# Kernel optimization log

Measured on AMD Instinct MI355X. Metric: run time of the kernel, lower is better.

## Reference

```python
import jax, jax.numpy as jnp
import numpy as np

BN_EPS = 1e-5


def setup_inputs() -> dict:
    key = jax.random.key(0)
    ks = jax.random.split(key, 11)
    C, P = 256, 128  # inplanes, planes = inplanes // 2
    B, H, W = 4, 64, 64
    s = 0.01  # conv weight init std in the original module
    return {
        "x": jax.random.normal(ks[0], (B, C, H, W), jnp.float32),
        "Wt": jax.random.normal(ks[1], (P, C), jnp.float32) * s,
        "bt": jnp.zeros((P,), jnp.float32),
        "Wp": jax.random.normal(ks[2], (P, C), jnp.float32) * s,
        "bp": jnp.zeros((P,), jnp.float32),
        "Wg": jax.random.normal(ks[3], (P, C), jnp.float32) * s,
        "bg": jnp.zeros((P,), jnp.float32),
        "Wz": jax.random.normal(ks[4], (C, P), jnp.float32) * s,
        "bz": jnp.zeros((C,), jnp.float32),
        "gamma": jax.random.uniform(ks[5], (C,), jnp.float32),
        "beta": jax.random.normal(ks[6], (C,), jnp.float32) * 0.01,
    }


def reference(x, Wt, bt, Wp, bp, Wg, bg, Wz, bz, gamma, beta):
    b, c, h, w = x.shape
    n = h * w
    xf = x.reshape(b, c, n)  # (b, c, n)
    # 1x1 conv projections == per-pixel matmuls
    t = jnp.einsum("pc,bcn->bnp", Wt, xf) + bt            # (b, n, p) queries
    p = jnp.einsum("pc,bcn->bpn", Wp, xf) + bp[:, None]   # (b, p, n) keys
    g = jnp.einsum("pc,bcn->bnp", Wg, xf) + bg            # (b, n, p) values
    planes = Wt.shape[0]
    scale = jnp.asarray(planes, x.dtype) ** 0.5
    att = jnp.einsum("bnp,bpm->bnm", t, p) / scale        # (b, n, n)
    att = jax.nn.softmax(att, axis=-1)                    # softmax over dim 2
    y = jnp.einsum("bnm,bmp->bnp", att, g)                # (b, n, p)
    z = jnp.einsum("cp,bnp->bcn", Wz, y) + bz[:, None]    # (b, c, n)
    z = z.reshape(b, c, h, w)
    # BatchNorm2d, training-mode batch statistics over (B, H, W)
    mean = z.mean(axis=(0, 2, 3))
    var = z.var(axis=(0, 2, 3))
    zn = (z - mean[:, None, None]) * jax.lax.rsqrt(var + BN_EPS)[:, None, None]
    out = zn * gamma[:, None, None] + beta[:, None, None] + x
    return out
```

## Files before the change

kernel.cpp:

```cpp
#include <hip/hip_runtime.h>


#define SCALE_ 0.08838834764831845f

typedef __bf16 bf16x8 __attribute__((ext_vector_type(8)));
typedef float f32x4 __attribute__((ext_vector_type(4)));
typedef unsigned short ushort8v __attribute__((ext_vector_type(8)));

__device__ inline unsigned short f2bf(float f) {
  unsigned int u = __float_as_uint(f);
  u += 0x7fffu + ((u >> 16) & 1u);
  return (unsigned short)(u >> 16);
}
__device__ inline float bflo(unsigned int u) { return __uint_as_float(u << 16); }
__device__ inline float bfhi(unsigned int u) { return __uint_as_float(u & 0xffff0000u); }

__device__ inline void gl16(const unsigned short* g, unsigned short* l) {
  __builtin_amdgcn_global_load_lds(
      (const __attribute__((address_space(1))) unsigned int*)(g),
      (__attribute__((address_space(3))) unsigned int*)(l), 16, 0, 0);
}

__global__ __launch_bounds__(256) void prep_kernel(
    const float* __restrict__ x,
    const float* __restrict__ Wt, const float* __restrict__ Wp, const float* __restrict__ Wg,
    unsigned short* __restrict__ xT, unsigned short* __restrict__ Wb) {
  const int tid = threadIdx.x;
  const int bx = blockIdx.x, b = blockIdx.y;
  if (bx >= 64) {
    if (b != 0) return;
#pragma unroll
    for (int it = 0; it < 3; ++it) {
      int k = (bx - 64) * 256 + tid + it * 4096;
      const float* src = (k < 4096 ? Wt : (k < 8192 ? Wp : Wg)) + (size_t)(k & 4095) * 8;
      float4 a = *(const float4*)src, c = *(const float4*)(src + 4);
      ushort8v us;
      us[0] = f2bf(a.x); us[1] = f2bf(a.y); us[2] = f2bf(a.z); us[3] = f2bf(a.w);
      us[4] = f2bf(c.x); us[5] = f2bf(c.y); us[6] = f2bf(c.z); us[7] = f2bf(c.w);
      *(ushort8v*)(Wb + (size_t)k * 8) = us;
    }
    return;
  }
  __shared__ float sT[128 * 68];
  const int w = tid >> 6, l = tid & 63;
  const int n0 = bx * 64;
  for (int half = 0; half < 2; ++half) {
    if (half) __syncthreads();
#pragma unroll
    for (int it = 0; it < 8; ++it) {
      int e = it * 256 + tid;
      int c = e >> 4, n4 = e & 15;
      float4 v = *(const float4*)(x + (size_t)(b * 256 + half * 128 + c) * 4096 + n0 + n4 * 4);
      *(float4*)(sT + c * 68 + n4 * 4) = v;
    }
    __syncthreads();
#pragma unroll
    for (int it = 0; it < 4; ++it) {
      int c8 = it * 4 + w;
      int n = l;
      ushort8v us;
#pragma unroll
      for (int j = 0; j < 8; ++j) us[j] = f2bf(sT[(c8 * 8 + j) * 68 + n]);
      *(ushort8v*)(xT + (size_t)b * 1048576 + (size_t)(n0 + n) * 256 + half * 128 + c8 * 8) = us;
    }
  }
}

__global__ __launch_bounds__(256, 3) void proj_kernel(
    const unsigned short* __restrict__ xT, const unsigned short* __restrict__ Wb,
    const float* __restrict__ bt, const float* __restrict__ bp, const float* __restrict__ bg,
    unsigned short* __restrict__ Qb, unsigned short* __restrict__ Kb,
    unsigned short* __restrict__ Vtb) {
  __shared__ unsigned short sX[64 * 256];
  __shared__ unsigned short sW[128 * 64];
  const int tid = threadIdx.x;
  const int w = tid >> 6, l = tid & 63;
  const int l15 = l & 15, lh = l >> 4;
  const int n0 = blockIdx.x * 64;
  const int b = blockIdx.y;
  const int sel = blockIdx.z;
  const unsigned short* xTb = xT + (size_t)b * 1048576;
  const unsigned short* Ws = Wb + (size_t)sel * 32768;
#pragma unroll
  for (int it = 0; it < 8; ++it) {
    int row = w * 16 + it * 2 + (l >> 5);
    int s = l & 31;
    int src = (s & 24) | ((s & 7) ^ (row & 7));
    gl16(xTb + (size_t)(n0 + row) * 256 + src * 8, sX + (w * 16 + it * 2) * 256);
  }
  f32x4 acc[2][4];
#pragma unroll
  for (int mt = 0; mt < 2; ++mt)
#pragma unroll
    for (int nt = 0; nt < 4; ++nt) acc[mt][nt] = (f32x4){0.f, 0.f, 0.f, 0.f};

  for (int ko4 = 0; ko4 < 4; ++ko4) {
    __syncthreads();
#pragma unroll
    for (int it = 0; it < 4; ++it) {
      int p = w * 32 + it * 8 + (l >> 3);
      int s = l & 7;
      gl16(Ws + (size_t)p * 256 + ko4 * 64 + ((s ^ (p & 7)) * 8),
           sW + (w * 32 + it * 8) * 64);
    }
    __syncthreads();
#pragma unroll
    for (int ko2 = 0; ko2 < 2; ++ko2) {
      bf16x8 af[2];
#pragma unroll
      for (int mt = 0; mt < 2; ++mt) {
        int p = w * 32 + mt * 16 + l15;
        af[mt] = *(const bf16x8*)(sW + p * 64 + (((ko2 * 4 + lh) ^ (p & 7)) << 3));
      }
#pragma unroll
      for (int nt = 0; nt < 4; ++nt) {
        int n = nt * 16 + l15;
        int ci = ko4 * 8 + ko2 * 4 + lh;
        int slot = (ci & 24) | ((ci & 7) ^ (n & 7));
        bf16x8 bfv = *(const bf16x8*)(sX + n * 256 + (slot << 3));
#pragma unroll
        for (int mt = 0; mt < 2; ++mt)
          acc[mt][nt] = __builtin_amdgcn_mfma_f32_16x16x32_bf16(af[mt], bfv, acc[mt][nt], 0, 0, 0);
      }
    }
  }
  const float* bias = sel == 0 ? bt : (sel == 1 ? bp : bg);
  const float scl = sel == 0 ? SCALE_ : 1.0f;
#pragma unroll
  for (int mt = 0; mt < 2; ++mt) {
    int pb = w * 32 + mt * 16 + lh * 4;
    float4 bv = *(const float4*)(bias + pb);
    const float* bvf = (const float*)&bv;
    if (sel < 2) {
      unsigned short* dst = (sel == 0 ? Qb : Kb) + (size_t)b * 524288;
#pragma unroll
      for (int nt = 0; nt < 4; ++nt) {
        ushort4 us;
        us.x = f2bf((acc[mt][nt][0] + bv.x) * scl);
        us.y = f2bf((acc[mt][nt][1] + bv.y) * scl);
        us.z = f2bf((acc[mt][nt][2] + bv.z) * scl);
        us.w = f2bf((acc[mt][nt][3] + bv.w) * scl);
        *(ushort4*)(dst + (size_t)(n0 + nt * 16 + l15) * 128 + pb) = us;
      }
    } else {
      unsigned short* dst = Vtb + (size_t)b * 524288;
#pragma unroll
      for (int nt = 0; nt < 4; ++nt)
#pragma unroll
        for (int r = 0; r < 4; ++r)
          dst[(size_t)(pb + r) * 4096 + n0 + nt * 16 + l15] = f2bf(acc[mt][nt][r] + bvf[r]);
    }
  }
}

__global__ __launch_bounds__(256, 4) void attn_kernel(
    const unsigned short* __restrict__ Qb, const unsigned short* __restrict__ Kb,
    const unsigned short* __restrict__ Vtb, unsigned short* __restrict__ Ytp,
    float* __restrict__ denp) {
  __shared__ unsigned short sm[18432];
  const int tid = threadIdx.x;
  const int w = tid >> 6, l = tid & 63;
  const int l15 = l & 15, lh = l >> 4;
  const int b = blockIdx.y, sp = blockIdx.z;
  const int n0 = blockIdx.x * 64;
  const int kvbase = sp * 1024;

  bf16x8 qf[4];
  {
    const unsigned short* qrow = Qb + (size_t)(b * 4096 + n0 + w * 16 + l15) * 128 + lh * 8;
#pragma unroll
    for (int ko = 0; ko < 4; ++ko) qf[ko] = *(const bf16x8*)(qrow + ko * 32);
  }
  unsigned short* sPw = sm + 16384 + w * 512;

  f32x4 yacc[8];
#pragma unroll
  for (int i = 0; i < 8; ++i) yacc[i] = (f32x4){0.f, 0.f, 0.f, 0.f};
  float den = 0.f;

  const unsigned short* Kbase = Kb + (size_t)(b * 4096 + kvbase) * 128;
  const unsigned short* Vbase = Vtb + (size_t)(b * 128) * 4096 + kvbase;

#define STAGE(T, BUFO)                                                              \
  {                                                                                 \
    const int koff_ = (T) * 32;                                                     \
    _Pragma("unroll")                                                               \
    for (int it = 0; it < 2; ++it) {                                                \
      int krow = w * 8 + it * 4 + (l >> 4);                                         \
      gl16(Kbase + (size_t)(koff_ + krow) * 128 + (((l & 15) ^ (krow & 7)) << 3),   \
           sm + (BUFO) + (w * 8 + it * 4) * 128);                                   \
      int vrow = w * 32 + it * 16 + (l >> 2);                                       \
      gl16(Vbase + (size_t)vrow * 4096 + koff_ + (((l & 3) ^ (vrow & 3)) << 3),     \
           sm + 8192 + (BUFO) + (w * 32 + it * 16) * 32);                           \
    }                                                                               \
  }

  STAGE(0, 0)
  for (int t = 0; t < 32; ++t) {
    const int co = (t & 1) * 4096;
    unsigned short* kb = sm + co;
    unsigned short* vb = sm + 8192 + co;
    __syncthreads();
    if (t + 1 < 32) {
      STAGE(t + 1, co ^ 4096)
    }
    f32x4 sacc[2];
#pragma unroll
    for (int mt = 0; mt < 2; ++mt) sacc[mt] = (f32x4){0.f, 0.f, 0.f, 0.f};
    __builtin_amdgcn_s_setprio(1);
#pragma unroll
    for (int ko = 0; ko < 4; ++ko) {
#pragma unroll
      for (int mt = 0; mt < 2; ++mt) {
        int m = mt * 16 + l15;
        bf16x8 ak = *(const bf16x8*)(kb + m * 128 + (((lh + 4 * ko) ^ (m & 7)) << 3));
        sacc[mt] = __builtin_amdgcn_mfma_f32_16x16x32_bf16(ak, qf[ko], sacc[mt], 0, 0, 0);
      }
    }
    __builtin_amdgcn_s_setprio(0);
    float rs = 0.f;
#pragma unroll
    for (int mt = 0; mt < 2; ++mt) {
      float e0 = __expf(sacc[mt][0]);
      float e1 = __expf(sacc[mt][1]);
      float e2 = __expf(sacc[mt][2]);
      float e3 = __expf(sacc[mt][3]);
      rs += (e0 + e1) + (e2 + e3);
      ushort4 us;
      us.x = f2bf(e0); us.y = f2bf(e1); us.z = f2bf(e2); us.w = f2bf(e3);
      int bk = mt * 2 + (lh >> 1);
      *(ushort4*)(sPw + l15 * 32 + ((bk ^ (l15 & 3)) << 3) + (lh & 1) * 4) = us;
    }
    rs += __shfl_xor(rs, 16);
    rs += __shfl_xor(rs, 32);
    den += rs;
    bf16x8 bp = *(const bf16x8*)(sPw + l15 * 32 + ((lh ^ (l15 & 3)) << 3));
    __builtin_amdgcn_s_setprio(1);
#pragma unroll
    for (int dt = 0; dt < 8; ++dt) {
      int d = dt * 16 + l15;
      bf16x8 av = *(const bf16x8*)(vb + d * 32 + ((lh ^ (d & 3)) << 3));
      yacc[dt] = __builtin_amdgcn_mfma_f32_16x16x32_bf16(av, bp, yacc[dt], 0, 0, 0);
    }
    __builtin_amdgcn_s_setprio(0);
  }
  unsigned short* Yt = Ytp + (size_t)(sp * 4 + b) * 524288 +
                       (size_t)(n0 + w * 16 + l15) * 128;
#pragma unroll
  for (int dt = 0; dt < 8; ++dt) {
    ushort4 us;
    us.x = f2bf(yacc[dt][0]); us.y = f2bf(yacc[dt][1]);
    us.z = f2bf(yacc[dt][2]); us.w = f2bf(yacc[dt][3]);
    *(ushort4*)(Yt + dt * 16 + lh * 4) = us;
  }
  if (lh == 0) denp[(size_t)(sp * 4 + b) * 4096 + n0 + w * 16 + l15] = den;
}

__global__ __launch_bounds__(256, 4) void zbn_kernel(
    const unsigned short* __restrict__ Ytp, const float* __restrict__ denp,
    const float* __restrict__ Wz, const float* __restrict__ bz,
    float* __restrict__ Z, float* __restrict__ S1p, float* __restrict__ S2p) {
  __shared__ unsigned short sY[64 * 128];
  __shared__ unsigned short sW[64 * 128];
  __shared__ float sDen[64];
  const int tid = threadIdx.x;
  const int w = tid >> 6, l = tid & 63;
  const int l15 = l & 15, lh = l >> 4;
  const int bx = blockIdx.x;
  const int b = blockIdx.y;
  const int n0 = bx * 64;
  const int c0 = blockIdx.z * 64;
  if (tid < 64) {
    float s = 0.f;
#pragma unroll
    for (int sp = 0; sp < 4; ++sp) s += denp[sp * 16384 + b * 4096 + n0 + tid];
    sDen[tid] = 1.0f / s;
  }
  __syncthreads();
#pragma unroll
  for (int it = 0; it < 4; ++it) {
    int e = it * 256 + tid;
    int n = e >> 4, pc = e & 15;
    size_t o = (size_t)b * 524288 + (size_t)(n0 + n) * 128 + pc * 8;
    float a0 = 0, a1 = 0, a2 = 0, a3 = 0, a4 = 0, a5 = 0, a6 = 0, a7 = 0;
#pragma unroll
    for (int sp = 0; sp < 4; ++sp) {
      uint4 v = *(const uint4*)(Ytp + (size_t)sp * 2097152 + o);
      a0 += bflo(v.x); a1 += bfhi(v.x);
      a2 += bflo(v.y); a3 += bfhi(v.y);
      a4 += bflo(v.z); a5 += bfhi(v.z);
      a6 += bflo(v.w); a7 += bfhi(v.w);
    }
    float idn = sDen[n];
    ushort8v us;
    us[0] = f2bf(a0 * idn); us[1] = f2bf(a1 * idn);
    us[2] = f2bf(a2 * idn); us[3] = f2bf(a3 * idn);
    us[4] = f2bf(a4 * idn); us[5] = f2bf(a5 * idn);
    us[6] = f2bf(a6 * idn); us[7] = f2bf(a7 * idn);
    *(ushort8v*)(sY + n * 128 + ((pc ^ (n & 7)) << 3)) = us;
  }
#pragma unroll
  for (int it = 0; it < 4; ++it) {
    int e = it * 256 + tid;
    int c = e >> 4, pc = e & 15;
    const float* wsrc = Wz + (size_t)(c0 + c) * 128 + pc * 8;
    float4 wa = *(const float4*)(wsrc);
    float4 wb = *(const float4*)(wsrc + 4);
    ushort8v us;
    us[0] = f2bf(wa.x); us[1] = f2bf(wa.y); us[2] = f2bf(wa.z); us[3] = f2bf(wa.w);
    us[4] = f2bf(wb.x); us[5] = f2bf(wb.y); us[6] = f2bf(wb.z); us[7] = f2bf(wb.w);
    *(ushort8v*)(sW + c * 128 + ((pc ^ (c & 7)) << 3)) = us;
  }
  __syncthreads();
  f32x4 acc[4];
#pragma unroll
  for (int nt = 0; nt < 4; ++nt) acc[nt] = (f32x4){0.f, 0.f, 0.f, 0.f};
  const int crow = w * 16 + l15;
#pragma unroll
  for (int ko = 0; ko < 4; ++ko) {
    bf16x8 aw = *(const bf16x8*)(sW + crow * 128 + (((lh + 4 * ko) ^ (crow & 7)) << 3));
#pragma unroll
    for (int nt = 0; nt < 4; ++nt) {
      int nrow = nt * 16 + l15;
      bf16x8 by = *(const bf16x8*)(sY + nrow * 128 + (((lh + 4 * ko) ^ (nrow & 7)) << 3));
      acc[nt] = __builtin_amdgcn_mfma_f32_16x16x32_bf16(aw, by, acc[nt], 0, 0, 0);
    }
  }
  const int cb = c0 + w * 16 + lh * 4;
  float4 bzv = *(const float4*)(bz + cb);
  const float* bzf = (const float*)&bzv;
#pragma unroll
  for (int r = 0; r < 4; ++r) {
    float s1 = 0.f, s2 = 0.f;
#pragma unroll
    for (int nt = 0; nt < 4; ++nt) {
      float z = acc[nt][r] + bzf[r];
      Z[(size_t)(b * 256 + cb + r) * 4096 + n0 + nt * 16 + l15] = z;
      s1 += z;
      s2 += z * z;
    }
#pragma unroll
    for (int m = 1; m < 16; m <<= 1) {
      s1 += __shfl_xor(s1, m);
      s2 += __shfl_xor(s2, m);
    }
    if (l15 == 0) {
      S1p[(size_t)(cb + r) * 256 + b * 64 + bx] = s1;
      S2p[(size_t)(cb + r) * 256 + b * 64 + bx] = s2;
    }
  }
}

__global__ __launch_bounds__(256) void bnfin_kernel(
    const float* __restrict__ S1p, const float* __restrict__ S2p,
    const float* __restrict__ gamma, const float* __restrict__ beta,
    float* __restrict__ Scale, float* __restrict__ Shift) {
  __shared__ float r1[4], r2[4];
  const int c = blockIdx.x, tid = threadIdx.x;
  float s1 = S1p[(size_t)c * 256 + tid];
  float s2 = S2p[(size_t)c * 256 + tid];
#pragma unroll
  for (int m = 1; m < 64; m <<= 1) {
    s1 += __shfl_xor(s1, m);
    s2 += __shfl_xor(s2, m);
  }
  if ((tid & 63) == 0) { r1[tid >> 6] = s1; r2[tid >> 6] = s2; }
  __syncthreads();
  if (tid == 0) {
    float S1t = (r1[0] + r1[1]) + (r1[2] + r1[3]);
    float S2t = (r2[0] + r2[1]) + (r2[2] + r2[3]);
    const float inv_cnt = 1.0f / 16384.0f;
    float mean = S1t * inv_cnt;
    float var = fmaxf(S2t * inv_cnt - mean * mean, 0.0f);
    float inv = rsqrtf(var + 1e-5f);
    float sc = gamma[c] * inv;
    Scale[c] = sc;
    Shift[c] = beta[c] - mean * sc;
  }
}

__global__ __launch_bounds__(256) void out_kernel(
    const float* __restrict__ Z, const float* __restrict__ x,
    const float* __restrict__ Scale, const float* __restrict__ Shift,
    float* __restrict__ out) {
  int i4 = blockIdx.x * 256 + threadIdx.x;
  int flat = i4 << 2;
  int c = (flat >> 12) & 255;
  float4 z = *(const float4*)(Z + flat);
  float4 xv = *(const float4*)(x + flat);
  float sc = Scale[c], sh = Shift[c];
  float4 o;
  o.x = z.x * sc + sh + xv.x;
  o.y = z.y * sc + sh + xv.y;
  o.z = z.z * sc + sh + xv.z;
  o.w = z.w * sc + sh + xv.w;
  *(float4*)(out + flat) = o;
}

extern "C" void kernel_launch(void* const* d_in, const int* in_sizes, int n_in,
                              void* d_out, int out_size, void* d_ws, size_t ws_size,
                              hipStream_t stream) {
  (void)in_sizes; (void)n_in; (void)out_size; (void)ws_size;
  const float* x = (const float*)d_in[0];
  const float* Wt = (const float*)d_in[1];
  const float* bt = (const float*)d_in[2];
  const float* Wp = (const float*)d_in[3];
  const float* bp = (const float*)d_in[4];
  const float* Wg = (const float*)d_in[5];
  const float* bg = (const float*)d_in[6];
  const float* Wz = (const float*)d_in[7];
  const float* bz = (const float*)d_in[8];
  const float* gamma = (const float*)d_in[9];
  const float* beta = (const float*)d_in[10];

  unsigned short* Qb = (unsigned short*)d_ws;
  unsigned short* Kb = Qb + 2097152;
  unsigned short* Vtb = Kb + 2097152;
  unsigned short* Ytp = Vtb + 2097152;
  float* denp = (float*)(Ytp + 8388608);
  float* Z = denp + 65536;
  float* Scale = Z + 4194304;
  float* Shift = Scale + 256;

  unsigned short* xT = (unsigned short*)Z;
  unsigned short* Wb = (unsigned short*)denp;
  float* S1p = (float*)Qb;
  float* S2p = S1p + 65536;

  prep_kernel<<<dim3(80, 4), 256, 0, stream>>>(x, Wt, Wp, Wg, xT, Wb);
  proj_kernel<<<dim3(64, 4, 3), 256, 0, stream>>>(xT, Wb, bt, bp, bg, Qb, Kb, Vtb);
  attn_kernel<<<dim3(64, 4, 4), 256, 0, stream>>>(Qb, Kb, Vtb, Ytp, denp);
  zbn_kernel<<<dim3(64, 4, 4), 256, 0, stream>>>(Ytp, denp, Wz, bz, Z, S1p, S2p);
  bnfin_kernel<<<256, 256, 0, stream>>>(S1p, S2p, gamma, beta, Scale, Shift);
  out_kernel<<<4096, 256, 0, stream>>>(Z, x, Scale, Shift, (float*)d_out);
}
```

Before: 100.7 us.

## Double query rows and KV tile per attention block to reuse staged K/V

Each attention block now handles 128 query rows (32 per wave, two 16-row sets) and stages 64 keys/values per iteration instead of 32, with wider swizzled LDS tiles. Every K and V fragment read from shared memory now feeds two MFMAs, and the loop runs 16 steps instead of 32, halving barrier count and global K/V traffic per query. In exchange it uses more registers and LDS, lowers the occupancy hint from 4 to 2 blocks, and launches half as many blocks (512), so there is less latency hiding and coarser work distribution across CUs.

```diff
diff --git a/kernel.cpp b/kernel.cpp
--- a/kernel.cpp
+++ b/kernel.cpp
@@ -153,107 +153,142 @@
   }
 }
 
-__global__ __launch_bounds__(256, 4) void attn_kernel(
+__global__ __launch_bounds__(256, 2) void attn_kernel(
     const unsigned short* __restrict__ Qb, const unsigned short* __restrict__ Kb,
     const unsigned short* __restrict__ Vtb, unsigned short* __restrict__ Ytp,
     float* __restrict__ denp) {
-  __shared__ unsigned short sm[18432];
+  __shared__ unsigned short sm[40960];
   const int tid = threadIdx.x;
   const int w = tid >> 6, l = tid & 63;
   const int l15 = l & 15, lh = l >> 4;
   const int b = blockIdx.y, sp = blockIdx.z;
-  const int n0 = blockIdx.x * 64;
+  const int n0 = blockIdx.x * 128;
   const int kvbase = sp * 1024;
 
-  bf16x8 qf[4];
+  bf16x8 qf0[4], qf1[4];
   {
-    const unsigned short* qrow = Qb + (size_t)(b * 4096 + n0 + w * 16 + l15) * 128 + lh * 8;
-#pragma unroll
-    for (int ko = 0; ko < 4; ++ko) qf[ko] = *(const bf16x8*)(qrow + ko * 32);
-  }
-  unsigned short* sPw = sm + 16384 + w * 512;
-
-  f32x4 yacc[8];
-#pragma unroll
-  for (int i = 0; i < 8; ++i) yacc[i] = (f32x4){0.f, 0.f, 0.f, 0.f};
-  float den = 0.f;
+    const unsigned short* q0 = Qb + (size_t)(b * 4096 + n0 + w * 32 + l15) * 128 + lh * 8;
+    const unsigned short* q1 = q0 + 16 * 128;
+#pragma unroll
+    for (int ko = 0; ko < 4; ++ko) {
+      qf0[ko] = *(const bf16x8*)(q0 + ko * 32);
+      qf1[ko] = *(const bf16x8*)(q1 + ko * 32);
+    }
+  }
+  unsigned short* sPw = sm + 32768 + w * 2048;
+
+  f32x4 yacc0[8], yacc1[8];
+#pragma unroll
+  for (int i = 0; i < 8; ++i) {
+    yacc0[i] = (f32x4){0.f, 0.f, 0.f, 0.f};
+    yacc1[i] = (f32x4){0.f, 0.f, 0.f, 0.f};
+  }
+  float den0 = 0.f, den1 = 0.f;
 
   const unsigned short* Kbase = Kb + (size_t)(b * 4096 + kvbase) * 128;
   const unsigned short* Vbase = Vtb + (size_t)(b * 128) * 4096 + kvbase;
 
 #define STAGE(T, BUFO)                                                              \
   {                                                                                 \
-    const int koff_ = (T) * 32;                                                     \
+    const int koff_ = (T) * 64;                                                     \
     _Pragma("unroll")                                                               \
-    for (int it = 0; it < 2; ++it) {                                                \
-      int krow = w * 8 + it * 4 + (l >> 4);                                         \
+    for (int it = 0; it < 4; ++it) {                                                \
+      int krow = w * 16 + it * 4 + (l >> 4);                                        \
       gl16(Kbase + (size_t)(koff_ + krow) * 128 + (((l & 15) ^ (krow & 7)) << 3),   \
-           sm + (BUFO) + (w * 8 + it * 4) * 128);                                   \
-      int vrow = w * 32 + it * 16 + (l >> 2);                                       \
-      gl16(Vbase + (size_t)vrow * 4096 + koff_ + (((l & 3) ^ (vrow & 3)) << 3),     \
-           sm + 8192 + (BUFO) + (w * 32 + it * 16) * 32);                           \
+           sm + (BUFO) + (w * 16 + it * 4) * 128);                                  \
+      int vrow = w * 32 + it * 8 + (l >> 3);                                        \
+      gl16(Vbase + (size_t)vrow * 4096 + koff_ + (((l & 7) ^ (vrow & 7)) << 3),     \
+           sm + 16384 + (BUFO) + (w * 32 + it * 8) * 64);                           \
     }                                                                               \
   }
 
   STAGE(0, 0)
-  for (int t = 0; t < 32; ++t) {
-    const int co = (t & 1) * 4096;
+  for (int t = 0; t < 16; ++t) {
+    const int co = (t & 1) * 8192;
     unsigned short* kb = sm + co;
-    unsigned short* vb = sm + 8192 + co;
+    unsigned short* vb = sm + 16384 + co;
     __syncthreads();
-    if (t + 1 < 32) {
-      STAGE(t + 1, co ^ 4096)
-    }
-    f32x4 sacc[2];
-#pragma unroll
-    for (int mt = 0; mt < 2; ++mt) sacc[mt] = (f32x4){0.f, 0.f, 0.f, 0.f};
+    if (t + 1 < 16) {
+      STAGE(t + 1, co ^ 8192)
+    }
+    f32x4 sacc0[4], sacc1[4];
+#pragma unroll
+    for (int mt = 0; mt < 4; ++mt) {
+      sacc0[mt] = (f32x4){0.f, 0.f, 0.f, 0.f};
+      sacc1[mt] = (f32x4){0.f, 0.f, 0.f, 0.f};
+    }
     __builtin_amdgcn_s_setprio(1);
 #pragma unroll
     for (int ko = 0; ko < 4; ++ko) {
 #pragma unroll
-      for (int mt = 0; mt < 2; ++mt) {
+      for (int mt = 0; mt < 4; ++mt) {
         int m = mt * 16 + l15;
         bf16x8 ak = *(const bf16x8*)(kb + m * 128 + (((lh + 4 * ko) ^ (m & 7)) << 3));
-        sacc[mt] = __builtin_amdgcn_mfma_f32_16x16x32_bf16(ak, qf[ko], sacc[mt], 0, 0, 0);
+        sacc0[mt] = __builtin_amdgcn_mfma_f32_16x16x32_bf16(ak, qf0[ko], sacc0[mt], 0, 0, 0);
+        sacc1[mt] = __builtin_amdgcn_mfma_f32_16x16x32_bf16(ak, qf1[ko], sacc1[mt], 0, 0, 0);
       }
     }
     __builtin_amdgcn_s_setprio(0);
-    float rs = 0.f;
-#pragma unroll
-    for (int mt = 0; mt < 2; ++mt) {
-      float e0 = __expf(sacc[mt][0]);
-      float e1 = __expf(sacc[mt][1]);
-      float e2 = __expf(sacc[mt][2]);
-      float e3 = __expf(sacc[mt][3]);
-      rs += (e0 + e1) + (e2 + e3);
+#define SOFTMAX_SET(SACC, ROWB, DEN)                                                \
+    {                                                                               \
+      float rs = 0.f;                                                               \
+      _Pragma("unroll")                                                             \
+      for (int mt = 0; mt < 4; ++mt) {                                              \
+        float e0 = __expf(SACC[mt][0]);                                             \
+        float e1 = __expf(SACC[mt][1]);                                             \
+        float e2 = __expf(SACC[mt][2]);                                             \
+        float e3 = __expf(SACC[mt][3]);                                             \
+        rs += (e0 + e1) + (e2 + e3);                                                \
+        ushort4 us;                                                                 \
+        us.x = f2bf(e0); us.y = f2bf(e1); us.z = f2bf(e2); us.w = f2bf(e3);         \
+        int mblk = mt * 2 + (lh >> 1);                                              \
+        *(ushort4*)(sPw + ((ROWB) + l15) * 64 + ((mblk ^ (l15 & 7)) << 3) +         \
+                    (lh & 1) * 4) = us;                                             \
+      }                                                                             \
+      rs += __shfl_xor(rs, 16);                                                     \
+      rs += __shfl_xor(rs, 32);                                                     \
+      DEN += rs;                                                                    \
+    }
+    SOFTMAX_SET(sacc0, 0, den0)
+    SOFTMAX_SET(sacc1, 16, den1)
+    __builtin_amdgcn_s_setprio(1);
+#pragma unroll
+    for (int ko = 0; ko < 2; ++ko) {
+      bf16x8 bp0 = *(const bf16x8*)(sPw + l15 * 64 + (((lh + 4 * ko) ^ (l15 & 7)) << 3));
+      bf16x8 bp1 = *(const bf16x8*)(sPw + (16 + l15) * 64 + (((lh + 4 * ko) ^ (l15 & 7)) << 3));
+#pragma unroll
+      for (int dt = 0; dt < 8; ++dt) {
+        int d = dt * 16 + l15;
+        bf16x8 av = *(const bf16x8*)(vb + d * 64 + (((lh + 4 * ko) ^ (d & 7)) << 3));
+        yacc0[dt] = __builtin_amdgcn_mfma_f32_16x16x32_bf16(av, bp0, yacc0[dt], 0, 0, 0);
+        yacc1[dt] = __builtin_amdgcn_mfma_f32_16x16x32_bf16(av, bp1, yacc1[dt], 0, 0, 0);
+      }
+    }
+    __builtin_amdgcn_s_setprio(0);
+  }
+  {
+    unsigned short* Yt = Ytp + (size_t)(sp * 4 + b) * 524288 +
+                         (size_t)(n0 + w * 32 + l15) * 128;
+#pragma unroll
+    for (int dt = 0; dt < 8; ++dt) {
       ushort4 us;
-      us.x = f2bf(e0); us.y = f2bf(e1); us.z = f2bf(e2); us.w = f2bf(e3);
-      int bk = mt * 2 + (lh >> 1);
-      *(ushort4*)(sPw + l15 * 32 + ((bk ^ (l15 & 3)) << 3) + (lh & 1) * 4) = us;
-    }
-    rs += __shfl_xor(rs, 16);
-    rs += __shfl_xor(rs, 32);
-    den += rs;
-    bf16x8 bp = *(const bf16x8*)(sPw + l15 * 32 + ((lh ^ (l15 & 3)) << 3));
-    __builtin_amdgcn_s_setprio(1);
+      us.x = f2bf(yacc0[dt][0]); us.y = f2bf(yacc0[dt][1]);
+      us.z = f2bf(yacc0[dt][2]); us.w = f2bf(yacc0[dt][3]);
+      *(ushort4*)(Yt + dt * 16 + lh * 4) = us;
+    }
+    unsigned short* Yt1 = Yt + 16 * 128;
 #pragma unroll
     for (int dt = 0; dt < 8; ++dt) {
-      int d = dt * 16 + l15;
-      bf16x8 av = *(const bf16x8*)(vb + d * 32 + ((lh ^ (d & 3)) << 3));
-      yacc[dt] = __builtin_amdgcn_mfma_f32_16x16x32_bf16(av, bp, yacc[dt], 0, 0, 0);
-    }
-    __builtin_amdgcn_s_setprio(0);
-  }
-  unsigned short* Yt = Ytp + (size_t)(sp * 4 + b) * 524288 +
-                       (size_t)(n0 + w * 16 + l15) * 128;
-#pragma unroll
-  for (int dt = 0; dt < 8; ++dt) {
-    ushort4 us;
-    us.x = f2bf(yacc[dt][0]); us.y = f2bf(yacc[dt][1]);
-    us.z = f2bf(yacc[dt][2]); us.w = f2bf(yacc[dt][3]);
-    *(ushort4*)(Yt + dt * 16 + lh * 4) = us;
-  }
-  if (lh == 0) denp[(size_t)(sp * 4 + b) * 4096 + n0 + w * 16 + l15] = den;
+      ushort4 us;
+      us.x = f2bf(yacc1[dt][0]); us.y = f2bf(yacc1[dt][1]);
+      us.z = f2bf(yacc1[dt][2]); us.w = f2bf(yacc1[dt][3]);
+      *(ushort4*)(Yt1 + dt * 16 + lh * 4) = us;
+    }
+    if (lh == 0) {
+      denp[(size_t)(sp * 4 + b) * 4096 + n0 + w * 32 + l15] = den0;
+      denp[(size_t)(sp * 4 + b) * 4096 + n0 + w * 32 + 16 + l15] = den1;
+    }
+  }
 }
 
 __global__ __launch_bounds__(256, 4) void zbn_kernel(
@@ -429,7 +464,7 @@
 
   prep_kernel<<<dim3(80, 4), 256, 0, stream>>>(x, Wt, Wp, Wg, xT, Wb);
   proj_kernel<<<dim3(64, 4, 3), 256, 0, stream>>>(xT, Wb, bt, bp, bg, Qb, Kb, Vtb);
-  attn_kernel<<<dim3(64, 4, 4), 256, 0, stream>>>(Qb, Kb, Vtb, Ytp, denp);
+  attn_kernel<<<dim3(32, 4, 4), 256, 0, stream>>>(Qb, Kb, Vtb, Ytp, denp);
   zbn_kernel<<<dim3(64, 4, 4), 256, 0, stream>>>(Ytp, denp, Wz, bz, Z, S1p, S2p);
   bnfin_kernel<<<256, 256, 0, stream>>>(S1p, S2p, gamma, beta, Scale, Shift);
   out_kernel<<<4096, 256, 0, stream>>>(Z, x, Scale, Shift, (float*)d_out);
```

Result: faster. 86.60 us (-14.0%).
